# Kernel optimization log

Measured on AMD Instinct MI355X. Metric: run time of the kernel, lower is better.

## Reference

```python
import jax, jax.numpy as jnp
import numpy as np

B, N, P = 64, 800000, 128          # batch, total CpG features, n_pathways (capsules)
H1, H2, C = 256, 128, 32           # MLP hidden_topology and n_output
EPS = 1e-5                         # BatchNorm1d eps


def _xavier(key, fan_in, fan_out, shape):
    bound = np.sqrt(6.0 / (fan_in + fan_out))
    return jax.random.uniform(key, shape, jnp.float32, -bound, bound)


def setup_inputs() -> dict:
    key = jax.random.key(0)
    ks = jax.random.split(key, 10)
    x = jax.random.normal(ks[0], (B, N), jnp.float32)
    # idx: sorted pathway assignment, equal capsule sizes N//P (matches module_lens)
    idx = jnp.sort(jax.random.randint(ks[1], (N,), 0, P)).astype(jnp.int64)
    # SPWModulesLayer.weight: xavier_uniform on shape (1, N)
    w = _xavier(ks[2], N, 1, (N,))
    co_w = jax.random.uniform(ks[3], (P,), jnp.float32, 0.0, 4.0)  # CancelOut init
    bn0_g, bn0_b = jnp.ones(P, jnp.float32), jnp.zeros(P, jnp.float32)
    W1, b1 = _xavier(ks[4], P, H1, (P, H1)), jnp.zeros(H1, jnp.float32)
    bn1_g, bn1_b = jnp.ones(H1, jnp.float32), jnp.zeros(H1, jnp.float32)
    W2, b2 = _xavier(ks[5], H1, H2, (H1, H2)), jnp.zeros(H2, jnp.float32)
    bn2_g, bn2_b = jnp.ones(H2, jnp.float32), jnp.zeros(H2, jnp.float32)
    Wo, bo = _xavier(ks[6], H2, C, (H2, C)), jnp.zeros(C, jnp.float32)
    return {"x": x, "w": w, "co_w": co_w,
            "bn0_g": bn0_g, "bn0_b": bn0_b,
            "W1": W1, "b1": b1, "bn1_g": bn1_g, "bn1_b": bn1_b,
            "W2": W2, "b2": b2, "bn2_g": bn2_g, "bn2_b": bn2_b,
            "Wo": Wo, "bo": bo, "idx": idx}


def _bn(z, g, b):
    # BatchNorm1d in training mode: batch mean, biased variance
    m = jnp.mean(z, axis=0)
    v = jnp.mean((z - m) ** 2, axis=0)
    return (z - m) * jax.lax.rsqrt(v + EPS) * g + b


def reference(x, w, co_w, bn0_g, bn0_b, W1, b1, bn1_g, bn1_b,
              W2, b2, bn2_g, bn2_b, Wo, bo, idx):
    # --- SPWModulesLayer: weighted scatter_add over pathway index (last dim) ---
    WX = jnp.zeros((x.shape[0], P), x.dtype).at[:, idx].add(x * w)   # [B, P]
    Z = _bn(jax.nn.relu(WX), bn0_g, bn0_b)                           # ReLU + BN
    Z = Z * jax.nn.sigmoid(co_w)                                     # CancelOut
    # --- MLP head: Linear->ReLU->BN twice, then Linear->Softmax ---
    h = _bn(jax.nn.relu(Z @ W1 + b1), bn1_g, bn1_b)
    h = _bn(jax.nn.relu(h @ W2 + b2), bn2_g, bn2_b)
    y = jax.nn.softmax(h @ Wo + bo, axis=-1)
    return (y, Z)
```

## Files before the change

### kernel.cpp

```cpp
#include <hip/hip_runtime.h>
#include <hip/hip_bf16.h>

#define BB     64
#define NF4    200000
#define CHUNKS 3125
#define NP     128
#define NH1    256
#define NH2    128
#define NC     32
#define EPSV   1e-5f

typedef float fx4 __attribute__((ext_vector_type(4)));

#define AS_G __attribute__((address_space(1)))
#define AS_L __attribute__((address_space(3)))

__device__ __forceinline__ float dot4(fx4 a, fx4 b) {
    return fmaf(a[0], b[0], fmaf(a[1], b[1], fmaf(a[2], b[2], a[3] * b[3])));
}

__global__ __launch_bounds__(64) void k_scatter(
    const float* __restrict__ x, const float* __restrict__ w,
    const int* __restrict__ idx, float* __restrict__ WX)
{
    __shared__ char lds[8 * 1024];
    const int lane = threadIdx.x;
    const int wid  = blockIdx.x;
    const int ch   = wid >> 1;
    const int bh   = (wid & 1) << 5;
    const int n4   = ch * 64 + lane;

    const fx4*  __restrict__ w4 = reinterpret_cast<const fx4*>(w);
    const int4* __restrict__ p4 = reinterpret_cast<const int4*>(idx);
    const fx4*  __restrict__ x4 = reinterpret_cast<const fx4*>(x);

    const fx4  wv = w4[n4];
    const int4 pv = p4[n4];
    const int  pLo = __builtin_amdgcn_readfirstlane(pv.x);
    const int  pHi = __shfl(pv.w, 63);
    const bool uniform = (pLo == pHi);

    fx4 wLo, wHi;
    wLo[0] = (pv.x == pLo) ? wv[0] : 0.f;  wHi[0] = (pv.x == pHi) ? wv[0] : 0.f;
    wLo[1] = (pv.y == pLo) ? wv[1] : 0.f;  wHi[1] = (pv.y == pHi) ? wv[1] : 0.f;
    wLo[2] = (pv.z == pLo) ? wv[2] : 0.f;  wHi[2] = (pv.z == pHi) ? wv[2] : 0.f;
    wLo[3] = (pv.w == pLo) ? wv[3] : 0.f;  wHi[3] = (pv.w == pHi) ? wv[3] : 0.f;

    #pragma unroll
    for (int i = 0; i < 7; ++i) {
        const float* gp = (const float*)(x4 + ((size_t)(bh + i) * NF4 + n4));
        __builtin_amdgcn_global_load_lds((const AS_G float*)gp,
                                         (AS_L float*)(lds + i * 1024), 16, 0, 0);
    }

    #pragma unroll
    for (int i = 0; i < 32; ++i) {
        if (i < 25) {
            asm volatile("s_waitcnt vmcnt(6)" ::: "memory");
        } else if (i == 25) {
            asm volatile("s_waitcnt vmcnt(0)" ::: "memory");
        }
        __builtin_amdgcn_sched_barrier(0);

        const fx4 xr = *reinterpret_cast<const fx4*>(lds + (i & 7) * 1024 + lane * 16);
        float sLo = dot4(xr, wLo);
        if (uniform) {
            #pragma unroll
            for (int off = 1; off < 64; off <<= 1)
                sLo += __shfl_xor(sLo, off);
            if (lane == 0)
                atomicAdd(&WX[(bh + i) * NP + pLo], sLo);
        } else {
            float sHi = dot4(xr, wHi);
            #pragma unroll
            for (int off = 1; off < 64; off <<= 1) {
                sLo += __shfl_xor(sLo, off);
                sHi += __shfl_xor(sHi, off);
            }
            if (lane == 0) {
                atomicAdd(&WX[(bh + i) * NP + pLo], sLo);
                atomicAdd(&WX[(bh + i) * NP + pHi], sHi);
            }
        }
        __builtin_amdgcn_sched_barrier(0);

        if (i < 25) {
            const float* gp = (const float*)(x4 + ((size_t)(bh + i + 7) * NF4 + n4));
            __builtin_amdgcn_global_load_lds((const AS_G float*)gp,
                                             (AS_L float*)(lds + ((i + 7) & 7) * 1024),
                                             16, 0, 0);
        }
        __builtin_amdgcn_sched_barrier(0);
    }
}

__global__ void k_bn0(const float* __restrict__ WX,
                      const float* __restrict__ co_w,
                      const float* __restrict__ g,
                      const float* __restrict__ beta,
                      float* __restrict__ Z)
{
    const int p = threadIdx.x;
    float sum = 0.f, sq = 0.f;
    for (int b = 0; b < BB; ++b) {
        float r = fmaxf(WX[b * NP + p], 0.f);
        sum += r; sq += r * r;
    }
    const float m   = sum * (1.f / BB);
    const float var = sq * (1.f / BB) - m * m;
    const float sc  = rsqrtf(var + EPSV) * g[p];
    const float bt  = beta[p];
    const float sig = 1.f / (1.f + expf(-co_w[p]));
    for (int b = 0; b < BB; ++b) {
        float r = fmaxf(WX[b * NP + p], 0.f);
        Z[b * NP + p] = ((r - m) * sc + bt) * sig;
    }
}

template <int K, int NOUT>
__global__ void k_fc_bn(const float* __restrict__ in,
                        const float* __restrict__ W,
                        const float* __restrict__ bias,
                        const float* __restrict__ g,
                        const float* __restrict__ beta,
                        float* __restrict__ out)
{
    const int j = blockIdx.x;
    const int b = threadIdx.x;
    const float* __restrict__ row = in + b * K;
    float acc = bias[j];
    #pragma unroll 8
    for (int k = 0; k < K; ++k)
        acc = fmaf(row[k], W[k * NOUT + j], acc);
    acc = fmaxf(acc, 0.f);
    float s = acc, q = acc * acc;
    #pragma unroll
    for (int off = 32; off > 0; off >>= 1) {
        s += __shfl_xor(s, off);
        q += __shfl_xor(q, off);
    }
    const float m   = s * (1.f / BB);
    const float var = q * (1.f / BB) - m * m;
    out[b * NOUT + j] = (acc - m) * rsqrtf(var + EPSV) * g[j] + beta[j];
}

__global__ void k_head(const float* __restrict__ h,
                       const float* __restrict__ Wo,
                       const float* __restrict__ bo,
                       float* __restrict__ y)
{
    const int b = blockIdx.x;
    const int c = threadIdx.x;
    const float* __restrict__ row = h + b * NH2;
    float acc = bo[c];
    #pragma unroll 8
    for (int k = 0; k < NH2; ++k)
        acc = fmaf(row[k], Wo[k * NC + c], acc);
    float mx = acc;
    #pragma unroll
    for (int off = 16; off > 0; off >>= 1)
        mx = fmaxf(mx, __shfl_xor(mx, off));
    const float e = expf(acc - mx);
    float s = e;
    #pragma unroll
    for (int off = 16; off > 0; off >>= 1)
        s += __shfl_xor(s, off);
    y[b * NC + c] = e / s;
}

extern "C" void kernel_launch(void* const* d_in, const int* in_sizes, int n_in,
                              void* d_out, int out_size, void* d_ws, size_t ws_size,
                              hipStream_t stream)
{
    const float* x    = (const float*)d_in[0];
    const float* w    = (const float*)d_in[1];
    const float* co_w = (const float*)d_in[2];
    const float* bn0g = (const float*)d_in[3];
    const float* bn0b = (const float*)d_in[4];
    const float* W1   = (const float*)d_in[5];
    const float* b1   = (const float*)d_in[6];
    const float* bn1g = (const float*)d_in[7];
    const float* bn1b = (const float*)d_in[8];
    const float* W2   = (const float*)d_in[9];
    const float* b2   = (const float*)d_in[10];
    const float* bn2g = (const float*)d_in[11];
    const float* bn2b = (const float*)d_in[12];
    const float* Wo   = (const float*)d_in[13];
    const float* bo   = (const float*)d_in[14];
    const int*   idx  = (const int*)d_in[15];

    float* out = (float*)d_out;
    float* y   = out;
    float* Z   = out + BB * NC;

    float* WX = (float*)d_ws;
    float* h1 = WX + BB * NP;
    float* h2 = h1 + BB * NH1;

    hipMemsetAsync(WX, 0, BB * NP * sizeof(float), stream);
    k_scatter<<<CHUNKS * 2, 64, 0, stream>>>(x, w, idx, WX);
    k_bn0<<<1, NP, 0, stream>>>(WX, co_w, bn0g, bn0b, Z);
    k_fc_bn<NP, NH1><<<NH1, BB, 0, stream>>>(Z, W1, b1, bn1g, bn1b, h1);
    k_fc_bn<NH1, NH2><<<NH2, BB, 0, stream>>>(h1, W2, b2, bn2g, bn2b, h2);
    k_head<<<BB, NC, 0, stream>>>(h2, Wo, bo, y);
}
```

Baseline: 89.10 us.

## Fuse BN0 and MLP head into one persistent kernel with grid barriers

Replaces the four small post-scatter kernels (BN0, two FC+BN layers, softmax head) with a single 64-block kernel that uses atomic-counter grid barriers between stages. Intermediates are stored transposed and staged through shared memory. The memset becomes a small zero kernel that also resets the barrier counters. This removes several launch gaps at the cost of spin-wait barriers, which assume all 64 blocks are co-resident.

```diff
diff --git a/kernel.cpp b/kernel.cpp
--- a/kernel.cpp
+++ b/kernel.cpp
@@ -9,6 +9,7 @@
 #define NH2    128
 #define NC     32
 #define EPSV   1e-5f
+#define NBLK   64
 
 typedef float fx4 __attribute__((ext_vector_type(4)));
 
@@ -94,46 +95,29 @@
     }
 }
 
-__global__ void k_bn0(const float* __restrict__ WX,
-                      const float* __restrict__ co_w,
-                      const float* __restrict__ g,
-                      const float* __restrict__ beta,
-                      float* __restrict__ Z)
-{
-    const int p = threadIdx.x;
-    float sum = 0.f, sq = 0.f;
-    for (int b = 0; b < BB; ++b) {
-        float r = fmaxf(WX[b * NP + p], 0.f);
-        sum += r; sq += r * r;
-    }
-    const float m   = sum * (1.f / BB);
-    const float var = sq * (1.f / BB) - m * m;
-    const float sc  = rsqrtf(var + EPSV) * g[p];
-    const float bt  = beta[p];
-    const float sig = 1.f / (1.f + expf(-co_w[p]));
-    for (int b = 0; b < BB; ++b) {
-        float r = fmaxf(WX[b * NP + p], 0.f);
-        Z[b * NP + p] = ((r - m) * sc + bt) * sig;
-    }
-}
-
-template <int K, int NOUT>
-__global__ void k_fc_bn(const float* __restrict__ in,
-                        const float* __restrict__ W,
-                        const float* __restrict__ bias,
-                        const float* __restrict__ g,
-                        const float* __restrict__ beta,
-                        float* __restrict__ out)
-{
-    const int j = blockIdx.x;
-    const int b = threadIdx.x;
-    const float* __restrict__ row = in + b * K;
-    float acc = bias[j];
-    #pragma unroll 8
-    for (int k = 0; k < K; ++k)
-        acc = fmaf(row[k], W[k * NOUT + j], acc);
-    acc = fmaxf(acc, 0.f);
-    float s = acc, q = acc * acc;
+__global__ void k_zero(float* __restrict__ WX, int* __restrict__ bar)
+{
+    const int i = blockIdx.x * 256 + threadIdx.x;
+    if (i < BB * NP) WX[i] = 0.f;
+    if (i < 8) bar[i] = 0;
+}
+
+__device__ __forceinline__ void gbar(int* c, int tid)
+{
+    __syncthreads();
+    if (tid == 0) {
+        __threadfence();
+        atomicAdd(c, 1);
+        while (__hip_atomic_load(c, __ATOMIC_ACQUIRE, __HIP_MEMORY_SCOPE_AGENT) < NBLK)
+            __builtin_amdgcn_s_sleep(2);
+    }
+    __syncthreads();
+    __threadfence();
+}
+
+__device__ __forceinline__ float bn_shfl(float a, float gj, float bj)
+{
+    float s = a, q = a * a;
     #pragma unroll
     for (int off = 32; off > 0; off >>= 1) {
         s += __shfl_xor(s, off);
@@ -141,31 +125,99 @@
     }
     const float m   = s * (1.f / BB);
     const float var = q * (1.f / BB) - m * m;
-    out[b * NOUT + j] = (acc - m) * rsqrtf(var + EPSV) * g[j] + beta[j];
-}
-
-__global__ void k_head(const float* __restrict__ h,
-                       const float* __restrict__ Wo,
-                       const float* __restrict__ bo,
-                       float* __restrict__ y)
-{
-    const int b = blockIdx.x;
-    const int c = threadIdx.x;
-    const float* __restrict__ row = h + b * NH2;
-    float acc = bo[c];
-    #pragma unroll 8
-    for (int k = 0; k < NH2; ++k)
-        acc = fmaf(row[k], Wo[k * NC + c], acc);
-    float mx = acc;
-    #pragma unroll
-    for (int off = 16; off > 0; off >>= 1)
-        mx = fmaxf(mx, __shfl_xor(mx, off));
-    const float e = expf(acc - mx);
-    float s = e;
-    #pragma unroll
-    for (int off = 16; off > 0; off >>= 1)
-        s += __shfl_xor(s, off);
-    y[b * NC + c] = e / s;
+    return (a - m) * rsqrtf(var + EPSV) * gj + bj;
+}
+
+__global__ __launch_bounds__(256) void k_head_fused(
+    const float* __restrict__ WX,   const float* __restrict__ co_w,
+    const float* __restrict__ bn0g, const float* __restrict__ bn0b,
+    const float* __restrict__ W1,   const float* __restrict__ b1,
+    const float* __restrict__ bn1g, const float* __restrict__ bn1b,
+    const float* __restrict__ W2,   const float* __restrict__ b2,
+    const float* __restrict__ bn2g, const float* __restrict__ bn2b,
+    const float* __restrict__ Wo,   const float* __restrict__ bo,
+    float* __restrict__ y, float* __restrict__ Zout,
+    float* __restrict__ Zt, float* __restrict__ h1t, float* __restrict__ h2t,
+    int* __restrict__ bar)
+{
+    __shared__ float buf[16384];
+    const int tid  = threadIdx.x;
+    const int wv   = tid >> 6;
+    const int lane = tid & 63;
+    const int blk  = blockIdx.x;
+
+    if (wv < 2) {
+        const int p = blk * 2 + wv;
+        const float r = fmaxf(WX[lane * NP + p], 0.f);
+        float s = r, q = r * r;
+        #pragma unroll
+        for (int off = 32; off > 0; off >>= 1) {
+            s += __shfl_xor(s, off);
+            q += __shfl_xor(q, off);
+        }
+        const float m   = s * (1.f / BB);
+        const float var = q * (1.f / BB) - m * m;
+        const float sig = 1.f / (1.f + expf(-co_w[p]));
+        const float z = ((r - m) * rsqrtf(var + EPSV) * bn0g[p] + bn0b[p]) * sig;
+        Zout[lane * NP + p] = z;
+        Zt[p * BB + lane]   = z;
+    }
+    gbar(&bar[0], tid);
+
+    #pragma unroll
+    for (int r = 0; r < 8; ++r) {
+        const int f4 = tid + 256 * r;
+        reinterpret_cast<fx4*>(buf)[f4] = reinterpret_cast<const fx4*>(Zt)[f4];
+    }
+    __syncthreads();
+    {
+        const int j = blk * 4 + wv;
+        float acc = b1[j];
+        #pragma unroll 8
+        for (int k = 0; k < NP; ++k)
+            acc = fmaf(buf[k * BB + lane], W1[k * NH1 + j], acc);
+        h1t[j * BB + lane] = bn_shfl(fmaxf(acc, 0.f), bn1g[j], bn1b[j]);
+    }
+    gbar(&bar[1], tid);
+
+    #pragma unroll
+    for (int r = 0; r < 16; ++r) {
+        const int f4 = tid + 256 * r;
+        reinterpret_cast<fx4*>(buf)[f4] = reinterpret_cast<const fx4*>(h1t)[f4];
+    }
+    __syncthreads();
+    if (wv < 2) {
+        const int j = blk * 2 + wv;
+        float acc = b2[j];
+        #pragma unroll 8
+        for (int k = 0; k < NH1; ++k)
+            acc = fmaf(buf[k * BB + lane], W2[k * NH2 + j], acc);
+        h2t[j * BB + lane] = bn_shfl(fmaxf(acc, 0.f), bn2g[j], bn2b[j]);
+    }
+    gbar(&bar[2], tid);
+
+    if (wv == 0) {
+        const int b  = blk;
+        const int c  = lane & 31;
+        const int kh = lane >> 5;
+        float acc = 0.f;
+        #pragma unroll 8
+        for (int k = kh * 64; k < kh * 64 + 64; ++k)
+            acc = fmaf(h2t[k * BB + b], Wo[k * NC + c], acc);
+        acc += __shfl_xor(acc, 32);
+        acc += bo[c];
+        float mx = acc;
+        #pragma unroll
+        for (int off = 16; off > 0; off >>= 1)
+            mx = fmaxf(mx, __shfl_xor(mx, off));
+        const float e = expf(acc - mx);
+        float sm = e;
+        #pragma unroll
+        for (int off = 16; off > 0; off >>= 1)
+            sm += __shfl_xor(sm, off);
+        if (lane < 32)
+            y[b * NC + c] = e / sm;
+    }
 }
 
 extern "C" void kernel_launch(void* const* d_in, const int* in_sizes, int n_in,
@@ -193,14 +245,16 @@
     float* y   = out;
     float* Z   = out + BB * NC;
 
-    float* WX = (float*)d_ws;
-    float* h1 = WX + BB * NP;
-    float* h2 = h1 + BB * NH1;
-
-    hipMemsetAsync(WX, 0, BB * NP * sizeof(float), stream);
+    float* WX  = (float*)d_ws;
+    float* Zt  = WX  + BB * NP;
+    float* h1t = Zt  + BB * NP;
+    float* h2t = h1t + BB * NH1;
+    int*   bar = (int*)(h2t + BB * NH2);
+
+    k_zero<<<32, 256, 0, stream>>>(WX, bar);
     k_scatter<<<CHUNKS * 2, 64, 0, stream>>>(x, w, idx, WX);
-    k_bn0<<<1, NP, 0, stream>>>(WX, co_w, bn0g, bn0b, Z);
-    k_fc_bn<NP, NH1><<<NH1, BB, 0, stream>>>(Z, W1, b1, bn1g, bn1b, h1);
-    k_fc_bn<NH1, NH2><<<NH2, BB, 0, stream>>>(h1, W2, b2, bn2g, bn2b, h2);
-    k_head<<<BB, NC, 0, stream>>>(h2, Wo, bo, y);
-}
+    k_head_fused<<<NBLK, 256, 0, stream>>>(WX, co_w, bn0g, bn0b,
+                                           W1, b1, bn1g, bn1b,
+                                           W2, b2, bn2g, bn2b,
+                                           Wo, bo, y, Z, Zt, h1t, h2t, bar);
+}
```

Result: slower. 102.3 us (+14.8%).
